# Kernel tuning notes

Measured on AMD Instinct MI355X. Metric: run time of the kernel, lower is better.

## Reference

```python
import jax, jax.numpy as jnp
import numpy as np

DROP_P = 0.5

def setup_inputs() -> dict:
    key = jax.random.key(0)
    k_x, k_q, k_k, k_v = jax.random.split(key, 4)
    T, d_in, d_out = 4096, 1024, 1024
    x = jax.random.normal(k_x, (T, d_in), dtype=jnp.float32)
    # torch nn.Linear weights are [d_out, d_in]; init scale ~ 1/sqrt(d_in)
    s = 1.0 / np.sqrt(d_in)
    W_query = jax.random.uniform(k_q, (d_out, d_in), jnp.float32, -s, s)
    W_key = jax.random.uniform(k_k, (d_out, d_in), jnp.float32, -s, s)
    W_value = jax.random.uniform(k_v, (d_out, d_in), jnp.float32, -s, s)
    return {"x": x, "W_query": W_query, "W_key": W_key, "W_value": W_value}


def reference(x, W_query, W_key, W_value):
    # QKV projections (y = x @ W.T, matching torch Linear)
    queries = x @ W_query.T          # [T, d]
    keys = x @ W_key.T               # [T, d]
    # values = x @ W_value.T  -> feeds only the unused context_vec; dead code omitted
    d = keys.shape[-1]
    T = x.shape[0]
    attn_scores = queries @ keys.T   # [T, T]
    attn_weights = jax.nn.softmax(attn_scores / jnp.sqrt(jnp.float32(d)), axis=-1)
    # post-softmax causal masking + row renormalization (as in source)
    row = jnp.arange(T)
    causal = (row[:, None] >= row[None, :]).astype(attn_weights.dtype)  # tril of ones
    masked = attn_weights * causal
    masked_norm = masked / jnp.sum(masked, axis=-1, keepdims=True)
    # dropout(p=0.5), train mode, fixed seed
    keep = jax.random.bernoulli(jax.random.key(123), 1.0 - DROP_P, masked_norm.shape)
    return jnp.where(keep, masked_norm / (1.0 - DROP_P), 0.0)
```

## Files before the change

kernel.cpp:

```cpp
#include <hip/hip_runtime.h>
#include <hip/hip_bf16.h>


using bf16   = __bf16;
using bf16x8 = __attribute__((ext_vector_type(8))) __bf16;
using bf16x4 = __attribute__((ext_vector_type(4))) __bf16;
using f32x4  = __attribute__((ext_vector_type(4))) float;

constexpr int Tdim = 4096;
constexpr int Ddim = 1024;

__global__ __launch_bounds__(256) void k_cast_bf16(const float* __restrict__ in,
                                                   bf16* __restrict__ out, int n4) {
  int i = blockIdx.x * 256 + threadIdx.x;
  if (i >= n4) return;
  f32x4 v = reinterpret_cast<const f32x4*>(in)[i];
  bf16x4 o;
  o[0] = (bf16)v[0]; o[1] = (bf16)v[1]; o[2] = (bf16)v[2]; o[3] = (bf16)v[3];
  reinterpret_cast<bf16x4*>(out)[i] = o;
}

__global__ __launch_bounds__(256) void k_tcast(const float* __restrict__ q,
                                               const float* __restrict__ k,
                                               bf16* __restrict__ qt,
                                               bf16* __restrict__ kt) {
  const float* in = blockIdx.z ? k : q;
  bf16* out = blockIdx.z ? kt : qt;
  __shared__ float t[32][33];
  const int tx = threadIdx.x & 31;
  const int ty = threadIdx.x >> 5;
  const int r0 = blockIdx.y * 32;
  const int c0 = blockIdx.x * 32;
#pragma unroll
  for (int r = 0; r < 4; ++r)
    t[ty * 4 + r][tx] = in[(r0 + ty * 4 + r) * Ddim + c0 + tx];
  __syncthreads();
#pragma unroll
  for (int r = 0; r < 4; ++r)
    out[(c0 + ty * 4 + r) * Ddim + r0 + tx] = (bf16)t[tx][ty * 4 + r];
}

__global__ __launch_bounds__(256) void k_redcast(const float* __restrict__ p,
                                                 bf16* __restrict__ g) {
  const int i = blockIdx.x * 256 + threadIdx.x;
  f32x4 a = reinterpret_cast<const f32x4*>(p)[i];
  f32x4 b = reinterpret_cast<const f32x4*>(p + (1 << 20))[i];
  f32x4 c = reinterpret_cast<const f32x4*>(p + (2 << 20))[i];
  f32x4 d = reinterpret_cast<const f32x4*>(p + (3 << 20))[i];
  f32x4 s = a + b + c + d;
  bf16x4 o;
  o[0] = (bf16)s[0]; o[1] = (bf16)s[1]; o[2] = (bf16)s[2]; o[3] = (bf16)s[3];
  reinterpret_cast<bf16x4*>(g)[i] = o;
}

__device__ __forceinline__ void gll16(const bf16* g, bf16* l) {
  __builtin_amdgcn_global_load_lds(
      (const __attribute__((address_space(1))) void*)g,
      (__attribute__((address_space(3))) void*)l, 16, 0, 0);
}

template<int OUTF32>
__global__ __launch_bounds__(256)
void k_gemm_bt(const bf16* __restrict__ A, const bf16* __restrict__ B,
               void* __restrict__ Cv, int N, int lda, int ldb, int kLen,
               long cZs, int causal) {
  const int nbn = N >> 7;
  const int bm = blockIdx.x / nbn;
  const int bn = blockIdx.x - bm * nbn;
  if (causal && bn > bm) return;

  __shared__ __align__(16) bf16 As[2][128 * 32];
  __shared__ __align__(16) bf16 Bs[2][128 * 32];

  const int tid  = threadIdx.x;
  const int lane = tid & 63;
  const int wid  = tid >> 6;
  const int wr   = (wid >> 1) * 64;
  const int wc   = (wid & 1) * 64;
  const int fr   = lane & 15;
  const int ko   = (lane >> 4) * 8;

  f32x4 acc[4][4];
#pragma unroll
  for (int i = 0; i < 4; ++i)
#pragma unroll
    for (int j = 0; j < 4; ++j) acc[i][j] = (f32x4){0.f, 0.f, 0.f, 0.f};

  const bf16* Ag = A + (long)bm * 128 * lda;
  const bf16* Bg = B + (long)bn * 128 * ldb;
  const int srow0 = tid >> 2;
  const int scol  = (tid & 3) * 8;
  const int k0 = blockIdx.y * kLen;

  auto stage = [&](int buf, int kt) {
#pragma unroll
    for (int i = 0; i < 2; ++i) {
      const int row = i * 64 + srow0;
      const int lb  = (i * 256 + wid * 64) * 8;
      gll16(Ag + (long)row * lda + kt + scol, &As[buf][lb]);
      gll16(Bg + (long)row * ldb + kt + scol, &Bs[buf][lb]);
    }
  };
  auto compute = [&](int buf) {
    bf16x8 av[4], bv[4];
#pragma unroll
    for (int f = 0; f < 4; ++f) {
      av[f] = *reinterpret_cast<const bf16x8*>(&As[buf][(wr + f * 16 + fr) * 32 + ko]);
      bv[f] = *reinterpret_cast<const bf16x8*>(&Bs[buf][(wc + f * 16 + fr) * 32 + ko]);
    }
#pragma unroll
    for (int fm = 0; fm < 4; ++fm)
#pragma unroll
      for (int fn = 0; fn < 4; ++fn)
        acc[fm][fn] = __builtin_amdgcn_mfma_f32_16x16x32_bf16(av[fm], bv[fn], acc[fm][fn], 0, 0, 0);
  };

  stage(0, k0);
  __syncthreads();
  int cur = 0;
  for (int kt = 32; kt < kLen; kt += 32) {
    stage(cur ^ 1, k0 + kt);
    compute(cur);
    __syncthreads();
    cur ^= 1;
  }
  compute(cur);

  const int crow0 = (lane >> 4) * 4;
  const int ccol  = lane & 15;
#pragma unroll
  for (int fm = 0; fm < 4; ++fm)
#pragma unroll
    for (int fn = 0; fn < 4; ++fn)
#pragma unroll
      for (int j = 0; j < 4; ++j) {
        const long row = (long)bm * 128 + wr + fm * 16 + crow0 + j;
        const long col = (long)bn * 128 + wc + fn * 16 + ccol;
        const float v = acc[fm][fn][j];
        if (OUTF32) ((float*)Cv + (long)blockIdx.y * cZs)[row * N + col] = v;
        else        ((bf16*)Cv)[row * N + col] = (bf16)v;
      }
}

__device__ __forceinline__ unsigned rotl32(unsigned v, int d) {
  return (v << d) | (v >> (32 - d));
}
__device__ __forceinline__ void threefry_123(unsigned x0, unsigned x1,
                                             unsigned& o0, unsigned& o1) {
  const unsigned ks0 = 0u, ks1 = 123u;
  const unsigned ks2 = 0x1BD11BDAu ^ ks0 ^ ks1;
  x0 += ks0; x1 += ks1;
#define TF_R4(a, b, c, d)                                   \
  x0 += x1; x1 = rotl32(x1, a); x1 ^= x0;                   \
  x0 += x1; x1 = rotl32(x1, b); x1 ^= x0;                   \
  x0 += x1; x1 = rotl32(x1, c); x1 ^= x0;                   \
  x0 += x1; x1 = rotl32(x1, d); x1 ^= x0;
  TF_R4(13, 15, 26, 6);  x0 += ks1; x1 += ks2 + 1u;
  TF_R4(17, 29, 16, 24); x0 += ks2; x1 += ks0 + 2u;
  TF_R4(13, 15, 26, 6);  x0 += ks0; x1 += ks1 + 3u;
  TF_R4(17, 29, 16, 24); x0 += ks1; x1 += ks2 + 4u;
  TF_R4(13, 15, 26, 6);  x0 += ks2; x1 += ks0 + 5u;
#undef TF_R4
  o0 = x0; o1 = x1;
}
__device__ __forceinline__ bool keep_bit(unsigned i) {
  unsigned o0, o1;
  threefry_123(0u, i, o0, o1);
  return ((o0 ^ o1) & 0x80000000u) == 0u;
}

__global__ __launch_bounds__(256) void k_softmax_drop(float* __restrict__ S) {
  const int b  = blockIdx.x;
  const int r0 = b, r1 = b + (Tdim / 2);
  const int tid = threadIdx.x;
  __shared__ float redA[4], redB[4];

  float v0[8], v1[16];
  float lm0 = -3.0e38f, lm1 = -3.0e38f;
#pragma unroll
  for (int i = 0; i < 8; ++i) {
    const int c = tid + i * 256;
    v0[i] = (c <= r0) ? S[(long)r0 * Tdim + c] : -3.0e38f;
    lm0 = fmaxf(lm0, v0[i]);
  }
#pragma unroll
  for (int i = 0; i < 16; ++i) {
    const int c = tid + i * 256;
    v1[i] = (c <= r1) ? S[(long)r1 * Tdim + c] : -3.0e38f;
    lm1 = fmaxf(lm1, v1[i]);
  }
#pragma unroll
  for (int o = 32; o; o >>= 1) {
    lm0 = fmaxf(lm0, __shfl_xor(lm0, o));
    lm1 = fmaxf(lm1, __shfl_xor(lm1, o));
  }
  if ((tid & 63) == 0) { redA[tid >> 6] = lm0; redB[tid >> 6] = lm1; }
  __syncthreads();
  const float m0 = fmaxf(fmaxf(redA[0], redA[1]), fmaxf(redA[2], redA[3]));
  const float m1 = fmaxf(fmaxf(redB[0], redB[1]), fmaxf(redB[2], redB[3]));
  __syncthreads();

  constexpr float SC = 1.0f / 32.0f;
  float ls0 = 0.f, ls1 = 0.f;
#pragma unroll
  for (int i = 0; i < 8; ++i) {
    const int c = tid + i * 256;
    const float e = (c <= r0) ? __expf((v0[i] - m0) * SC) : 0.f;
    v0[i] = e; ls0 += e;
  }
#pragma unroll
  for (int i = 0; i < 16; ++i) {
    const int c = tid + i * 256;
    const float e = (c <= r1) ? __expf((v1[i] - m1) * SC) : 0.f;
    v1[i] = e; ls1 += e;
  }
#pragma unroll
  for (int o = 32; o; o >>= 1) { ls0 += __shfl_xor(ls0, o); ls1 += __shfl_xor(ls1, o); }
  if ((tid & 63) == 0) { redA[tid >> 6] = ls0; redB[tid >> 6] = ls1; }
  __syncthreads();
  const float inv0 = 2.0f / (redA[0] + redA[1] + redA[2] + redA[3]);
  const float inv1 = 2.0f / (redB[0] + redB[1] + redB[2] + redB[3]);

#pragma unroll
  for (int i = 0; i < 16; ++i) {
    const int c = tid + i * 256;
    const unsigned j = (unsigned)(r0 * Tdim + c);
    float o1v = 0.f;
    if (c <= r1 && keep_bit(j + 8388608u)) o1v = v1[i] * inv1;
    S[(long)r1 * Tdim + c] = o1v;
    float o0v = 0.f;
    if (i < 8 && c <= r0 && keep_bit(j)) o0v = v0[i & 7] * inv0;
    S[(long)r0 * Tdim + c] = o0v;
  }
}

extern "C" void kernel_launch(void* const* d_in, const int* in_sizes, int n_in,
                              void* d_out, int out_size, void* d_ws, size_t ws_size,
                              hipStream_t stream) {
  const float* x  = (const float*)d_in[0];
  const float* Wq = (const float*)d_in[1];
  const float* Wk = (const float*)d_in[2];
  float* S = (float*)d_out;
  char* ws = (char*)d_ws;
  bf16*  xb = (bf16*)(ws);
  bf16*  qt = (bf16*)(ws + (8l  << 20));
  bf16*  kt = (bf16*)(ws + (10l << 20));
  float* Wp = (float*)(ws + (12l << 20));
  bf16*  G  = (bf16*)(ws + (28l << 20));
  bf16*  P  = (bf16*)(ws + (30l << 20));

  k_cast_bf16<<<(Tdim * Ddim / 4) / 256, 256, 0, stream>>>(x, xb, Tdim * Ddim / 4);
  k_tcast<<<dim3(32, 32, 2), 256, 0, stream>>>(Wq, Wk, qt, kt);

  k_gemm_bt<1><<<dim3(64, 4), 256, 0, stream>>>(kt, qt, (void*)Wp, Ddim, Ddim, Ddim,
                                                Ddim / 4, 1l << 20, 0);
  k_redcast<<<(Ddim * Ddim / 4) / 256, 256, 0, stream>>>(Wp, G);

  k_gemm_bt<0><<<dim3((Tdim / 128) * (Ddim / 128), 1), 256, 0, stream>>>(
      xb, G, (void*)P, Ddim, Ddim, Ddim, Ddim, 0, 0);
  k_gemm_bt<1><<<dim3((Tdim / 128) * (Tdim / 128), 1), 256, 0, stream>>>(
      P, xb, (void*)S, Tdim, Ddim, Ddim, Ddim, 0, 1);

  k_softmax_drop<<<Tdim / 2, 256, 0, stream>>>(S);
}
```

Before: 193.7 us.

## Use 512-thread GEMM with intra-block split-K, XCD swizzle, vectorized softmax

The bf16 GEMM kernel now runs 8 waves per block. Two groups of four waves each handle half of a 64-wide K tile, and their partial accumulators are summed through an LDS reduction buffer that shares storage with the tiles. It also remaps block indices in groups of 8, presumably so neighbouring tiles land on the same XCD for L2 reuse, and raises wave priority around the MFMA loop. The softmax/dropout kernel switches to contiguous 16-column-per-thread f32x4 loads and stores, and only the first 128 threads do work for the shorter row. The aim is fewer loop iterations and barriers per K, better cache locality and wider memory accesses, at the cost of more LDS per block, possibly lower occupancy and an extra reduction step.

```diff
diff --git a/kernel.cpp b/kernel.cpp
--- a/kernel.cpp
+++ b/kernel.cpp
@@ -60,25 +60,35 @@
 }
 
 template<int OUTF32>
-__global__ __launch_bounds__(256)
-void k_gemm_bt(const bf16* __restrict__ A, const bf16* __restrict__ B,
-               void* __restrict__ Cv, int N, int lda, int ldb, int kLen,
-               long cZs, int causal) {
+__global__ __launch_bounds__(512)
+void k_gemm8(const bf16* __restrict__ A, const bf16* __restrict__ B,
+             void* __restrict__ Cv, int N, int lda, int ldb, int kLen,
+             long cZs, int causal) {
+  union SMem {
+    bf16  t[2][2][128 * 64];
+    float red[256 * 65];
+  };
+  __shared__ SMem sm;
+
   const int nbn = N >> 7;
-  const int bm = blockIdx.x / nbn;
-  const int bn = blockIdx.x - bm * nbn;
+  int bx = blockIdx.x;
+  {
+    const int cpx = gridDim.x >> 3;
+    bx = (bx & 7) * cpx + (bx >> 3);
+  }
+  const int bm = bx / nbn;
+  const int bn = bx - bm * nbn;
   if (causal && bn > bm) return;
-
-  __shared__ __align__(16) bf16 As[2][128 * 32];
-  __shared__ __align__(16) bf16 Bs[2][128 * 32];
 
   const int tid  = threadIdx.x;
   const int lane = tid & 63;
   const int wid  = tid >> 6;
-  const int wr   = (wid >> 1) * 64;
-  const int wc   = (wid & 1) * 64;
+  const int g    = wid >> 2;
+  const int w2   = wid & 3;
+  const int wr   = (w2 >> 1) * 64;
+  const int wc   = (w2 & 1) * 64;
   const int fr   = lane & 15;
-  const int ko   = (lane >> 4) * 8;
+  const int ko   = g * 32 + (lane >> 4) * 8;
 
   f32x4 acc[4][4];
 #pragma unroll
@@ -88,58 +98,73 @@
 
   const bf16* Ag = A + (long)bm * 128 * lda;
   const bf16* Bg = B + (long)bn * 128 * ldb;
-  const int srow0 = tid >> 2;
-  const int scol  = (tid & 3) * 8;
   const int k0 = blockIdx.y * kLen;
 
+  const int r1_ = tid >> 3,          cb1 = (tid & 7) * 8;
+  const int r2_ = (tid + 512) >> 3,  cb2 = (tid & 7) * 8;
+
   auto stage = [&](int buf, int kt) {
-#pragma unroll
-    for (int i = 0; i < 2; ++i) {
-      const int row = i * 64 + srow0;
-      const int lb  = (i * 256 + wid * 64) * 8;
-      gll16(Ag + (long)row * lda + kt + scol, &As[buf][lb]);
-      gll16(Bg + (long)row * ldb + kt + scol, &Bs[buf][lb]);
-    }
+    gll16(Ag + (long)r1_ * lda + kt + cb1, &sm.t[buf][0][tid * 8]);
+    gll16(Bg + (long)r1_ * ldb + kt + cb1, &sm.t[buf][1][tid * 8]);
+    gll16(Ag + (long)r2_ * lda + kt + cb2, &sm.t[buf][0][(tid + 512) * 8]);
+    gll16(Bg + (long)r2_ * ldb + kt + cb2, &sm.t[buf][1][(tid + 512) * 8]);
   };
   auto compute = [&](int buf) {
     bf16x8 av[4], bv[4];
 #pragma unroll
     for (int f = 0; f < 4; ++f) {
-      av[f] = *reinterpret_cast<const bf16x8*>(&As[buf][(wr + f * 16 + fr) * 32 + ko]);
-      bv[f] = *reinterpret_cast<const bf16x8*>(&Bs[buf][(wc + f * 16 + fr) * 32 + ko]);
-    }
+      av[f] = *reinterpret_cast<const bf16x8*>(&sm.t[buf][0][(wr + f * 16 + fr) * 64 + ko]);
+      bv[f] = *reinterpret_cast<const bf16x8*>(&sm.t[buf][1][(wc + f * 16 + fr) * 64 + ko]);
+    }
+    __builtin_amdgcn_s_setprio(1);
 #pragma unroll
     for (int fm = 0; fm < 4; ++fm)
 #pragma unroll
       for (int fn = 0; fn < 4; ++fn)
         acc[fm][fn] = __builtin_amdgcn_mfma_f32_16x16x32_bf16(av[fm], bv[fn], acc[fm][fn], 0, 0, 0);
+    __builtin_amdgcn_s_setprio(0);
   };
 
+  const int nIter = kLen >> 6;
   stage(0, k0);
   __syncthreads();
   int cur = 0;
-  for (int kt = 32; kt < kLen; kt += 32) {
-    stage(cur ^ 1, k0 + kt);
+  for (int it = 1; it < nIter; ++it) {
+    stage(cur ^ 1, k0 + it * 64);
     compute(cur);
     __syncthreads();
     cur ^= 1;
   }
   compute(cur);
 
-  const int crow0 = (lane >> 4) * 4;
-  const int ccol  = lane & 15;
-#pragma unroll
-  for (int fm = 0; fm < 4; ++fm)
-#pragma unroll
-    for (int fn = 0; fn < 4; ++fn)
-#pragma unroll
-      for (int j = 0; j < 4; ++j) {
-        const long row = (long)bm * 128 + wr + fm * 16 + crow0 + j;
-        const long col = (long)bn * 128 + wc + fn * 16 + ccol;
-        const float v = acc[fm][fn][j];
-        if (OUTF32) ((float*)Cv + (long)blockIdx.y * cZs)[row * N + col] = v;
-        else        ((bf16*)Cv)[row * N + col] = (bf16)v;
-      }
+  __syncthreads();
+  const int rrow = w2 * 64 + lane;
+  if (g == 1) {
+#pragma unroll
+    for (int fm = 0; fm < 4; ++fm)
+#pragma unroll
+      for (int fn = 0; fn < 4; ++fn)
+#pragma unroll
+        for (int j = 0; j < 4; ++j)
+          sm.red[rrow * 65 + fm * 16 + fn * 4 + j] = acc[fm][fn][j];
+  }
+  __syncthreads();
+  if (g == 0) {
+    const int crow0 = (lane >> 4) * 4;
+    const int ccol  = lane & 15;
+#pragma unroll
+    for (int fm = 0; fm < 4; ++fm)
+#pragma unroll
+      for (int fn = 0; fn < 4; ++fn)
+#pragma unroll
+        for (int j = 0; j < 4; ++j) {
+          const float v = acc[fm][fn][j] + sm.red[rrow * 65 + fm * 16 + fn * 4 + j];
+          const long row = (long)bm * 128 + wr + fm * 16 + crow0 + j;
+          const long col = (long)bn * 128 + wc + fn * 16 + ccol;
+          if (OUTF32) ((float*)Cv + (long)blockIdx.y * cZs)[row * N + col] = v;
+          else        ((bf16*)Cv)[row * N + col] = (bf16)v;
+        }
+  }
 }
 
 __device__ __forceinline__ unsigned rotl32(unsigned v, int d) {
@@ -173,21 +198,39 @@
   const int b  = blockIdx.x;
   const int r0 = b, r1 = b + (Tdim / 2);
   const int tid = threadIdx.x;
+  const int cb  = tid * 16;
   __shared__ float redA[4], redB[4];
 
-  float v0[8], v1[16];
+  float* row0 = S + (long)r0 * Tdim;
+  float* row1 = S + (long)r1 * Tdim;
+
+  f32x4 v1[4], v0[4];
   float lm0 = -3.0e38f, lm1 = -3.0e38f;
 #pragma unroll
-  for (int i = 0; i < 8; ++i) {
-    const int c = tid + i * 256;
-    v0[i] = (c <= r0) ? S[(long)r0 * Tdim + c] : -3.0e38f;
-    lm0 = fmaxf(lm0, v0[i]);
-  }
-#pragma unroll
-  for (int i = 0; i < 16; ++i) {
-    const int c = tid + i * 256;
-    v1[i] = (c <= r1) ? S[(long)r1 * Tdim + c] : -3.0e38f;
-    lm1 = fmaxf(lm1, v1[i]);
+  for (int i = 0; i < 4; ++i) {
+    const int c = cb + i * 4;
+    f32x4 v = (c <= r1) ? *reinterpret_cast<const f32x4*>(row1 + c)
+                        : (f32x4){0.f, 0.f, 0.f, 0.f};
+#pragma unroll
+    for (int l = 0; l < 4; ++l) {
+      if (c + l > r1) v[l] = -3.0e38f;
+      lm1 = fmaxf(lm1, v[l]);
+    }
+    v1[i] = v;
+  }
+  if (tid < 128) {
+#pragma unroll
+    for (int i = 0; i < 4; ++i) {
+      const int c = cb + i * 4;
+      f32x4 v = (c <= r0) ? *reinterpret_cast<const f32x4*>(row0 + c)
+                          : (f32x4){0.f, 0.f, 0.f, 0.f};
+#pragma unroll
+      for (int l = 0; l < 4; ++l) {
+        if (c + l > r0) v[l] = -3.0e38f;
+        lm0 = fmaxf(lm0, v[l]);
+      }
+      v0[i] = v;
+    }
   }
 #pragma unroll
   for (int o = 32; o; o >>= 1) {
@@ -203,16 +246,26 @@
   constexpr float SC = 1.0f / 32.0f;
   float ls0 = 0.f, ls1 = 0.f;
 #pragma unroll
-  for (int i = 0; i < 8; ++i) {
-    const int c = tid + i * 256;
-    const float e = (c <= r0) ? __expf((v0[i] - m0) * SC) : 0.f;
-    v0[i] = e; ls0 += e;
-  }
-#pragma unroll
-  for (int i = 0; i < 16; ++i) {
-    const int c = tid + i * 256;
-    const float e = (c <= r1) ? __expf((v1[i] - m1) * SC) : 0.f;
-    v1[i] = e; ls1 += e;
+  for (int i = 0; i < 4; ++i) {
+#pragma unroll
+    for (int l = 0; l < 4; ++l) {
+      const int c = cb + i * 4 + l;
+      float e = 0.f;
+      if (c <= r1) { e = __expf((v1[i][l] - m1) * SC); ls1 += e; }
+      v1[i][l] = e;
+    }
+  }
+  if (tid < 128) {
+#pragma unroll
+    for (int i = 0; i < 4; ++i) {
+#pragma unroll
+      for (int l = 0; l < 4; ++l) {
+        const int c = cb + i * 4 + l;
+        float e = 0.f;
+        if (c <= r0) { e = __expf((v0[i][l] - m0) * SC); ls0 += e; }
+        v0[i][l] = e;
+      }
+    }
   }
 #pragma unroll
   for (int o = 32; o; o >>= 1) { ls0 += __shfl_xor(ls0, o); ls1 += __shfl_xor(ls1, o); }
@@ -222,15 +275,24 @@
   const float inv1 = 2.0f / (redB[0] + redB[1] + redB[2] + redB[3]);
 
 #pragma unroll
-  for (int i = 0; i < 16; ++i) {
-    const int c = tid + i * 256;
-    const unsigned j = (unsigned)(r0 * Tdim + c);
-    float o1v = 0.f;
-    if (c <= r1 && keep_bit(j + 8388608u)) o1v = v1[i] * inv1;
-    S[(long)r1 * Tdim + c] = o1v;
-    float o0v = 0.f;
-    if (i < 8 && c <= r0 && keep_bit(j)) o0v = v0[i & 7] * inv0;
-    S[(long)r0 * Tdim + c] = o0v;
+  for (int i = 0; i < 4; ++i) {
+    const int c = cb + i * 4;
+    f32x4 o1v = {0.f, 0.f, 0.f, 0.f};
+#pragma unroll
+    for (int l = 0; l < 4; ++l) {
+      const int cc = c + l;
+      if (cc <= r1 && keep_bit((unsigned)(r1 * Tdim + cc))) o1v[l] = v1[i][l] * inv1;
+    }
+    *reinterpret_cast<f32x4*>(row1 + c) = o1v;
+    f32x4 o0v = {0.f, 0.f, 0.f, 0.f};
+    if (tid < 128) {
+#pragma unroll
+      for (int l = 0; l < 4; ++l) {
+        const int cc = c + l;
+        if (cc <= r0 && keep_bit((unsigned)(r0 * Tdim + cc))) o0v[l] = v0[i][l] * inv0;
+      }
+    }
+    *reinterpret_cast<f32x4*>(row0 + c) = o0v;
   }
 }
 
@@ -252,14 +314,14 @@
   k_cast_bf16<<<(Tdim * Ddim / 4) / 256, 256, 0, stream>>>(x, xb, Tdim * Ddim / 4);
   k_tcast<<<dim3(32, 32, 2), 256, 0, stream>>>(Wq, Wk, qt, kt);
 
-  k_gemm_bt<1><<<dim3(64, 4), 256, 0, stream>>>(kt, qt, (void*)Wp, Ddim, Ddim, Ddim,
-                                                Ddim / 4, 1l << 20, 0);
+  k_gemm8<1><<<dim3(64, 4), 512, 0, stream>>>(kt, qt, (void*)Wp, Ddim, Ddim, Ddim,
+                                              Ddim / 4, 1l << 20, 0);
   k_redcast<<<(Ddim * Ddim / 4) / 256, 256, 0, stream>>>(Wp, G);
 
-  k_gemm_bt<0><<<dim3((Tdim / 128) * (Ddim / 128), 1), 256, 0, stream>>>(
-      xb, G, (void*)P, Ddim, Ddim, Ddim, Ddim, 0, 0);
-  k_gemm_bt<1><<<dim3((Tdim / 128) * (Tdim / 128), 1), 256, 0, stream>>>(
-      P, xb, (void*)S, Tdim, Ddim, Ddim, Ddim, 0, 1);
+  k_gemm8<0><<<dim3(256, 1), 512, 0, stream>>>(xb, G, (void*)P, Ddim, Ddim, Ddim,
+                                               Ddim, 0, 0);
+  k_gemm8<1><<<dim3(1024, 1), 512, 0, stream>>>(P, xb, (void*)S, Tdim, Ddim, Ddim,
+                                                Ddim, 0, 1);
 
   k_softmax_drop<<<Tdim / 2, 256, 0, stream>>>(S);
 }
```

New measurement: 464.8 us. +140.0%, slower.
